# Performance work log

Hardware: AMD Instinct MI355X
Metric: run time of the kernel (lower is better)

## Reference

```python
import jax, jax.numpy as jnp
import numpy as np

N = 25000   # num nodes
E = 500000  # num edges
B = 4       # num queries (batch)
D = 32      # hidden dim
R2 = 474    # doubled num_relation
L = 4       # num conv layers
EPS = 1e-6


def setup_inputs() -> dict:
    key = jax.random.key(0)
    ks = jax.random.split(key, 12)
    return {
        "node_in": jax.random.randint(ks[0], (E,), 0, N),
        "node_out": jax.random.randint(ks[1], (E,), 0, N),
        "relation": jax.random.randint(ks[2], (E,), 0, R2),
        "edge_weight": jnp.ones((E,), jnp.float32),
        "h_index": jax.random.randint(ks[3], (B,), 0, N),
        "r_index": jax.random.randint(ks[4], (B,), 0, R2),
        "query_embed": jax.random.normal(ks[5], (R2, D), jnp.float32) * 0.1,
        "rel_W": jax.random.normal(ks[6], (L, D, R2 * D), jnp.float32) * 0.05,
        "rel_b": jnp.zeros((L, R2 * D), jnp.float32),
        "lin_W": jax.random.normal(ks[7], (L, 13 * D, D), jnp.float32) * 0.05,
        "lin_b": jnp.zeros((L, D), jnp.float32),
        "mlp_W1": jax.random.normal(ks[8], (2 * D, 2 * D), jnp.float32) * 0.05,
        "mlp_b1": jnp.zeros((2 * D,), jnp.float32),
        "mlp_W2": jax.random.normal(ks[9], (2 * D, 1), jnp.float32) * 0.05,
        "mlp_b2": jnp.zeros((1,), jnp.float32),
    }


def _nbfnet(node_in, node_out, relation, h_index, r_index,
            edge_weight, query_embed, rel_W, rel_b, lin_W, lin_b,
            mlp_W1, mlp_b1, mlp_W2, mlp_b2):
    query = query_embed[r_index]                                   # [B, D]
    # boundary condition: query embedding placed at the head node of each query
    boundary = jnp.zeros((N, B, D), query.dtype).at[h_index, jnp.arange(B)].set(query)
    # append one self-entry per node (boundary message), as in the torch code
    node_out_ext = jnp.concatenate([node_out, jnp.arange(N)])      # [E+N]
    w_ext = jnp.concatenate([edge_weight, jnp.ones((N,), edge_weight.dtype)])[:, None, None]
    cnt = jax.ops.segment_sum(jnp.ones((E + N,), query.dtype), node_out_ext, N)[:, None, None]
    deg = jax.ops.segment_sum(edge_weight, node_out, N) + 1.0      # degree_out + 1, [N]
    scale = jnp.log(deg)
    scale = scale / scale.mean()
    scales = jnp.stack([jnp.ones_like(scale), scale, 1.0 / jnp.clip(scale, 0.01)], -1)  # [N,3]

    hidden = boundary
    for l in range(L):
        # dependent relation embeddings: [R2, B, D]
        rel_in = (query @ rel_W[l] + rel_b[l]).reshape(B, R2, D).transpose(1, 0, 2)
        # distmult message + boundary self-message: [E+N, B, D]
        msg = jnp.concatenate([rel_in[relation] * hidden[node_in], boundary], 0)
        mw = msg * w_ext
        mean = jax.ops.segment_sum(mw, node_out_ext, N) / cnt
        sq_mean = jax.ops.segment_sum(msg * mw, node_out_ext, N) / cnt
        mx = jax.ops.segment_max(mw, node_out_ext, N)
        mn = jax.ops.segment_min(mw, node_out_ext, N)
        std = jnp.sqrt(jnp.clip(sq_mean - mean * mean, EPS))
        feat = jnp.stack([mean, mx, mn, std], -1).reshape(N, B, 4 * D)   # PNA stats
        update = (feat[..., None] * scales[:, None, None, :]).reshape(N, B, 12 * D)
        hidden = jax.nn.relu(jnp.concatenate([hidden, update], -1) @ lin_W[l] + lin_b[l])

    feat = jnp.concatenate([hidden, jnp.broadcast_to(query[None], (N, B, D))], -1)  # [N,B,2D]
    h1 = jax.nn.relu(feat @ mlp_W1 + mlp_b1)
    score = (h1 @ mlp_W2 + mlp_b2)[..., 0]                          # [N, B]
    return score.T                                                  # [B, N]


def reference(node_in, node_out, relation, edge_weight, h_index, r_index,
              query_embed, rel_W, rel_b, lin_W, lin_b,
              mlp_W1, mlp_b1, mlp_W2, mlp_b2):
    return _nbfnet(node_in, node_out, relation, h_index, r_index,
                   edge_weight, query_embed, rel_W, rel_b, lin_W, lin_b,
                   mlp_W1, mlp_b1, mlp_W2, mlp_b2)
```

## Files before the change

### kernel.cpp

```cpp
#include <hip/hip_runtime.h>
#include <hip/hip_fp16.h>

#define NN  25000
#define EE  500000
#define BB  4
#define DD  32
#define LL  4
#define R2C 474
#define BD  128
#define THD 416
#define EPSF 1e-6f
#define WMH 13312

typedef _Float16 half8 __attribute__((ext_vector_type(8)));
typedef float    f32x4 __attribute__((ext_vector_type(4)));

__global__ __launch_bounds__(256) void pidx_kernel(const int4* __restrict__ no4,
                                                   int* __restrict__ cnt,
                                                   int4* __restrict__ pidx4) {
  int i = blockIdx.x * 256 + threadIdx.x;
  if (i >= EE / 4) return;
  int4 d = no4[i];
  int4 r;
  r.x = atomicAdd(&cnt[d.x], 1);
  r.y = atomicAdd(&cnt[d.y], 1);
  r.z = atomicAdd(&cnt[d.z], 1);
  r.w = atomicAdd(&cnt[d.w], 1);
  pidx4[i] = r;
}

__global__ __launch_bounds__(256) void prep_kernel(const int* __restrict__ cnt,
                                                   int* __restrict__ base,
                                                   int* __restrict__ gcnt) {
  int n = blockIdx.x * 256 + threadIdx.x;
  if (n >= NN) return;
  base[n] = atomicAdd(gcnt, (cnt[n] + 1) & ~1);
}

__global__ __launch_bounds__(256) void scatter_kernel(const int4* __restrict__ ni4,
                                                      const int4* __restrict__ no4,
                                                      const int4* __restrict__ rl4,
                                                      const float4* __restrict__ ew4,
                                                      const int* __restrict__ base,
                                                      const int4* __restrict__ pidx4,
                                                      int2* __restrict__ ep) {
  int i = blockIdx.x * 256 + threadIdx.x;
  if (i >= EE / 4) return;
  int4 ni = ni4[i], no = no4[i], rl = rl4[i], pi = pidx4[i];
  float4 w = ew4[i];
  ep[base[no.x] + pi.x] = make_int2(ni.x | (rl.x << 15), __float_as_int(w.x));
  ep[base[no.y] + pi.y] = make_int2(ni.y | (rl.y << 15), __float_as_int(w.y));
  ep[base[no.z] + pi.z] = make_int2(ni.z | (rl.z << 15), __float_as_int(w.z));
  ep[base[no.w] + pi.w] = make_int2(ni.w | (rl.w << 15), __float_as_int(w.w));
}

__global__ __launch_bounds__(256) void wdeg_kernel(const int* __restrict__ base,
                                                   const int* __restrict__ cnt,
                                                   const int2* __restrict__ ep,
                                                   float* __restrict__ lg,
                                                   float* __restrict__ logsum) {
  int n = blockIdx.x * 256 + threadIdx.x;
  float v = 0.f;
  if (n < NN) {
    int b = base[n], c = cnt[n];
    float s = 0.f;
    for (int p = b; p < b + c; ++p) s += __int_as_float(ep[p].y);
    v = logf(s + 1.0f);
    lg[n] = v;
  }
  __shared__ float red[256];
  red[threadIdx.x] = v; __syncthreads();
  for (int o = 128; o > 0; o >>= 1) {
    if (threadIdx.x < o) red[threadIdx.x] += red[threadIdx.x + o];
    __syncthreads();
  }
  if (threadIdx.x == 0) atomicAdd(logsum, red[0]);
}

__global__ __launch_bounds__(128) void init_kernel(const int* __restrict__ r_index,
                                                   const float* __restrict__ qemb,
                                                   float* __restrict__ query) {
  int t = threadIdx.x; int b = t >> 5, d = t & 31;
  query[t] = qemb[r_index[b] * DD + d];
}

__global__ __launch_bounds__(256) void relin_all_kernel(const float* __restrict__ query,
                                                        const float* __restrict__ relW,
                                                        const float* __restrict__ relB,
                                                        __half* __restrict__ relIn) {
  int o = blockIdx.x * 256 + threadIdx.x;
  if (o >= LL * R2C * BD) return;
  int l = o / (R2C * BD);
  int rest = o % (R2C * BD);
  int r = rest >> 7, b = (rest >> 5) & 3, d = rest & 31;
  int col = r * DD + d;
  const float* W = relW + (size_t)l * DD * R2C * DD;
  float acc = relB[(size_t)l * R2C * DD + col];
  #pragma unroll
  for (int k = 0; k < DD; ++k)
    acc = fmaf(query[b * DD + k], W[(size_t)k * (R2C * DD) + col], acc);
  relIn[o] = __float2half(acc);
}

__global__ __launch_bounds__(256) void wmbuild_kernel(const float* __restrict__ linW,
                                                      _Float16* __restrict__ Wm) {
  int idx = blockIdx.x * 256 + threadIdx.x;
  if (idx >= LL * WMH) return;
  int l = idx / WMH, rest = idx % WMH;
  int t = rest >> 10;
  int nt = (rest >> 9) & 1;
  int L = (rest >> 3) & 63;
  int j = rest & 7;
  int k = t * 32 + (L >> 4) * 8 + j;
  int n = nt * 16 + (L & 15);
  int wrow;
  if (k < 32) wrow = k;
  else {
    int kk = k - 32;
    int slab = kk >> 7, s = (kk >> 5) & 3, dd = kk & 31;
    wrow = DD + (dd * 4 + s) * 3 + slab;
  }
  Wm[idx] = (_Float16)linW[(size_t)l * THD * DD + (size_t)wrow * DD + n];
}

__device__ __forceinline__ void mfma_epilogue(const _Float16* sh,
                                              const _Float16* hinh,
                                              __half* houth,
                                              const float* lg,
                                              const float* logsum,
                                              const _Float16* Wm,
                                              const float* bias,
                                              const float* query,
                                              const int* h_index,
                                              int nbase, int lane, bool hzero) {
  const int m = lane & 15;
  const int q = lane >> 4;
  const int nl = m >> 2;
  const int n = nbase + nl;
  const int b = m & 3;
  const float sc = lg[n] * ((float)NN / logsum[0]);
  const _Float16 one = (_Float16)1.f;
  const _Float16 s1h = (_Float16)sc;
  const _Float16 s2h = (_Float16)(1.0f / fmaxf(sc, 0.01f));
  const _Float16* ssrc = sh + nl * 512 + b * 32 + q * 8;

  f32x4 c0 = {0.f, 0.f, 0.f, 0.f};
  f32x4 c1 = {0.f, 0.f, 0.f, 0.f};
  half8 a;
  if (hzero) {
    a = (half8)(_Float16)0.f;
    if (n == h_index[b]) {
      const float* qp = query + b * 32 + q * 8;
      #pragma unroll
      for (int j = 0; j < 8; ++j) a[j] = (_Float16)qp[j];
    }
  } else {
    a = *(const half8*)(hinh + (unsigned)n * BD + b * 32 + q * 8);
  }
  #pragma unroll
  for (int t = 0; t < 13; ++t) {
    if (t > 0) {
      const int slab = (t - 1) >> 2, s = (t - 1) & 3;
      a = *(const half8*)(ssrc + s * 128);
      const _Float16 sch = (slab == 0) ? one : ((slab == 1) ? s1h : s2h);
      half8 sv = {sch, sch, sch, sch, sch, sch, sch, sch};
      a = a * sv;
    }
    half8 b0 = *(const half8*)(Wm + (unsigned)(t * 2 + 0) * 512 + lane * 8);
    half8 b1 = *(const half8*)(Wm + (unsigned)(t * 2 + 1) * 512 + lane * 8);
    c0 = __builtin_amdgcn_mfma_f32_16x16x32_f16(a, b0, c0, 0, 0, 0);
    c1 = __builtin_amdgcn_mfma_f32_16x16x32_f16(a, b1, c1, 0, 0, 0);
  }
  const int col = lane & 15;
  const float bj0 = bias[col], bj1 = bias[col + 16];
  #pragma unroll
  for (int i = 0; i < 4; ++i) {
    const int mr = q * 4 + i;
    __half* dst = houth + (unsigned)(nbase + (mr >> 2)) * BD + (mr & 3) * 32 + col;
    dst[0]  = __float2half(fmaxf(c0[i] + bj0, 0.f));
    dst[16] = __float2half(fmaxf(c1[i] + bj1, 0.f));
  }
}

__global__ __launch_bounds__(256) void layer1_fused_kernel(
    const __half2* __restrict__ rel2, const int2* __restrict__ ep,
    const int* __restrict__ base, const int* __restrict__ cnt,
    const int* __restrict__ h_index, const float* __restrict__ query,
    const float* __restrict__ lg, const float* __restrict__ logsum,
    const _Float16* __restrict__ Wm, const float* __restrict__ bias,
    __half* __restrict__ houth) {
  __shared__ __align__(16) __half2 sh[4][256];
  const int lane = threadIdx.x & 63;
  const int wid  = threadIdx.x >> 6;
  const int nbase = blockIdx.x * 4;
  const int n = nbase + wid;
  const int b = lane >> 4;
  const int d0 = (lane & 15) * 2;
  const float q0 = query[b * 32 + d0], q1 = query[b * 32 + d0 + 1];
  const int hb = h_index[b];
  const int beg = __builtin_amdgcn_readfirstlane(base[n]);
  const int cnn = __builtin_amdgcn_readfirstlane(cnt[n]);
  const float mb0 = (n == hb) ? q0 : 0.f;
  const float mb1 = (n == hb) ? q1 : 0.f;
  float sa0 = mb0, qa0 = mb0 * mb0, mx0 = mb0, mn0 = mb0;
  float sa1 = mb1, qa1 = mb1 * mb1, mx1 = mb1, mn1 = mb1;
  int matched = 0;
  for (int p = beg; p < beg + cnn; ++p) {
    int2 e = ep[p];
    if ((e.x & 0x7fff) == hb) {
      __half2 rv = rel2[(unsigned)((unsigned)e.x >> 15) * 64 + lane];
      float w = __int_as_float(e.y);
      float2 rf = __half22float2(rv);
      float m0 = rf.x * q0, mw0 = m0 * w;
      float m1 = rf.y * q1, mw1 = m1 * w;
      sa0 += mw0; qa0 = fmaf(m0, mw0, qa0); mx0 = fmaxf(mx0, mw0); mn0 = fminf(mn0, mw0);
      sa1 += mw1; qa1 = fmaf(m1, mw1, qa1); mx1 = fmaxf(mx1, mw1); mn1 = fminf(mn1, mw1);
      ++matched;
    }
  }
  if (matched < cnn) {
    mx0 = fmaxf(mx0, 0.f); mn0 = fminf(mn0, 0.f);
    mx1 = fmaxf(mx1, 0.f); mn1 = fminf(mn1, 0.f);
  }
  const float invc = 1.0f / (float)(cnn + 1);
  const float mean0 = sa0 * invc, mean1 = sa1 * invc;
  const float sd0 = sqrtf(fmaxf(qa0 * invc - mean0 * mean0, EPSF));
  const float sd1 = sqrtf(fmaxf(qa1 * invc - mean1 * mean1, EPSF));
  sh[wid][lane]       = __floats2half2_rn(mean0, mean1);
  sh[wid][64 + lane]  = __floats2half2_rn(mx0, mx1);
  sh[wid][128 + lane] = __floats2half2_rn(mn0, mn1);
  sh[wid][192 + lane] = __floats2half2_rn(sd0, sd1);
  __syncthreads();
  if (threadIdx.x >= 64) return;
  mfma_epilogue((const _Float16*)&sh[0][0], nullptr, houth, lg, logsum,
                Wm, bias, query, h_index, nbase, lane, true);
}

__global__ __launch_bounds__(256) void layer_fused_kernel(
    const __half2* __restrict__ hin2, const __half2* __restrict__ rel2,
    const int2* __restrict__ ep, const int* __restrict__ base,
    const int* __restrict__ cnt, const int* __restrict__ h_index,
    const float* __restrict__ query, const float* __restrict__ lg,
    const float* __restrict__ logsum, const _Float16* __restrict__ Wm,
    const float* __restrict__ bias, __half* __restrict__ houth) {
  __shared__ __align__(16) __half2 sh[4][256];
  const int lane = threadIdx.x & 63;
  const int wid  = threadIdx.x >> 6;
  const int nbase = blockIdx.x * 4;
  const int n = nbase + wid;
  const int b = lane >> 4;
  const int d0 = (lane & 15) * 2;
  const float q0 = query[b * 32 + d0], q1 = query[b * 32 + d0 + 1];
  const int hb = h_index[b];
  const int beg = __builtin_amdgcn_readfirstlane(base[n]);
  const int cnn = __builtin_amdgcn_readfirstlane(cnt[n]);
  const float mb0 = (n == hb) ? q0 : 0.f;
  const float mb1 = (n == hb) ? q1 : 0.f;
  float sa0 = mb0, qa0 = mb0 * mb0, mx0 = mb0, mn0 = mb0;
  float sa1 = mb1, qa1 = mb1 * mb1, mx1 = mb1, mn1 = mb1;

#define PROC(Ez, Hv, Rv) {                                                   \
    float w = __int_as_float(Ez);                                            \
    float2 hf = __half22float2(Hv), rf = __half22float2(Rv);                 \
    float m0 = rf.x * hf.x, mw0 = m0 * w;                                    \
    float m1 = rf.y * hf.y, mw1 = m1 * w;                                    \
    sa0 += mw0; qa0 = fmaf(m0, mw0, qa0);                                    \
    mx0 = fmaxf(mx0, mw0); mn0 = fminf(mn0, mw0);                            \
    sa1 += mw1; qa1 = fmaf(m1, mw1, qa1);                                    \
    mx1 = fmaxf(mx1, mw1); mn1 = fminf(mn1, mw1); }
#define ROWS(Ex, Hd, Rd) {                                                   \
    Hd = hin2[(unsigned)((Ex) & 0x7fff) * 64 + lane];                        \
    Rd = rel2[(unsigned)((unsigned)(Ex) >> 15) * 64 + lane]; }

  int p = beg;
  int rem = cnn;
  const int nb = rem >> 3;
  if (nb > 0) {
    int2 E0, E1, E2, E3, E4, E5, E6, E7;
    __half2 H0, H1, H2, H3, H4, H5, H6, H7;
    __half2 R0, R1, R2, R3, R4, R5, R6, R7;
    E0 = ep[p];     E1 = ep[p + 1]; E2 = ep[p + 2]; E3 = ep[p + 3];
    E4 = ep[p + 4]; E5 = ep[p + 5]; E6 = ep[p + 6]; E7 = ep[p + 7];
    ROWS(E0.x, H0, R0); ROWS(E1.x, H1, R1); ROWS(E2.x, H2, R2); ROWS(E3.x, H3, R3);
    ROWS(E4.x, H4, R4); ROWS(E5.x, H5, R5); ROWS(E6.x, H6, R6); ROWS(E7.x, H7, R7);
    for (int it = 1; it < nb; ++it) {
      const int pn = p + 8;
      int2 F0 = ep[pn],     F1 = ep[pn + 1], F2 = ep[pn + 2], F3 = ep[pn + 3];
      int2 F4 = ep[pn + 4], F5 = ep[pn + 5], F6 = ep[pn + 6], F7 = ep[pn + 7];
      __half2 G0, G1, G2, G3, G4, G5, G6, G7;
      __half2 S0, S1, S2, S3, S4, S5, S6, S7;
      ROWS(F0.x, G0, S0); ROWS(F1.x, G1, S1); ROWS(F2.x, G2, S2); ROWS(F3.x, G3, S3);
      ROWS(F4.x, G4, S4); ROWS(F5.x, G5, S5); ROWS(F6.x, G6, S6); ROWS(F7.x, G7, S7);
      PROC(E0.y, H0, R0); PROC(E1.y, H1, R1); PROC(E2.y, H2, R2); PROC(E3.y, H3, R3);
      PROC(E4.y, H4, R4); PROC(E5.y, H5, R5); PROC(E6.y, H6, R6); PROC(E7.y, H7, R7);
      E0 = F0; E1 = F1; E2 = F2; E3 = F3; E4 = F4; E5 = F5; E6 = F6; E7 = F7;
      H0 = G0; H1 = G1; H2 = G2; H3 = G3; H4 = G4; H5 = G5; H6 = G6; H7 = G7;
      R0 = S0; R1 = S1; R2 = S2; R3 = S3; R4 = S4; R5 = S5; R6 = S6; R7 = S7;
      p = pn;
    }
    PROC(E0.y, H0, R0); PROC(E1.y, H1, R1); PROC(E2.y, H2, R2); PROC(E3.y, H3, R3);
    PROC(E4.y, H4, R4); PROC(E5.y, H5, R5); PROC(E6.y, H6, R6); PROC(E7.y, H7, R7);
    p += 8;
    rem -= nb << 3;
  }
  if (rem >= 4) {
    int2 E0 = ep[p], E1 = ep[p + 1], E2 = ep[p + 2], E3 = ep[p + 3];
    __half2 H0, H1, H2, H3, R0, R1, R2, R3;
    ROWS(E0.x, H0, R0); ROWS(E1.x, H1, R1); ROWS(E2.x, H2, R2); ROWS(E3.x, H3, R3);
    PROC(E0.y, H0, R0); PROC(E1.y, H1, R1); PROC(E2.y, H2, R2); PROC(E3.y, H3, R3);
    p += 4; rem -= 4;
  }
  for (; rem > 0; --rem, ++p) {
    int2 e = ep[p];
    __half2 hv, rv;
    ROWS(e.x, hv, rv);
    PROC(e.y, hv, rv);
  }
#undef ROWS
#undef PROC
  const float invc = 1.0f / (float)(cnn + 1);
  const float mean0 = sa0 * invc, mean1 = sa1 * invc;
  const float sd0 = sqrtf(fmaxf(qa0 * invc - mean0 * mean0, EPSF));
  const float sd1 = sqrtf(fmaxf(qa1 * invc - mean1 * mean1, EPSF));
  sh[wid][lane]       = __floats2half2_rn(mean0, mean1);
  sh[wid][64 + lane]  = __floats2half2_rn(mx0, mx1);
  sh[wid][128 + lane] = __floats2half2_rn(mn0, mn1);
  sh[wid][192 + lane] = __floats2half2_rn(sd0, sd1);
  __syncthreads();
  if (threadIdx.x >= 64) return;
  mfma_epilogue((const _Float16*)&sh[0][0], (const _Float16*)hin2, houth,
                lg, logsum, Wm, bias, query, h_index, nbase, lane, false);
}

__global__ __launch_bounds__(128) void mlp_kernel(const __half* __restrict__ hinh,
                                                  const float* __restrict__ query,
                                                  const float* __restrict__ W1,
                                                  const float* __restrict__ b1,
                                                  const float* __restrict__ W2,
                                                  const float* __restrict__ b2,
                                                  float* __restrict__ out) {
  __shared__ float f2[BB][2 * DD];
  const int t = threadIdx.x;
  const int b = t >> 5, d = t & 31;
  const float qv = query[t];
  const float w2a = W2[d], w2b = W2[DD + d];
  const float b1a = b1[d], b1b = b1[DD + d];
  const float b2v = b2[0];
  const int NPBM = 8;
  int n0 = blockIdx.x * NPBM, n1 = min(n0 + NPBM, NN);
  for (int n = n0; n < n1; ++n) {
    f2[b][d]      = __half2float(hinh[(unsigned)n * BD + t]);
    f2[b][DD + d] = qv;
    float a0 = b1a, a1 = b1b;
    #pragma unroll
    for (int i = 0; i < 2 * DD; ++i) {
      float v = f2[b][i];
      a0 = fmaf(v, W1[i * 2 * DD + d], a0);
      a1 = fmaf(v, W1[i * 2 * DD + DD + d], a1);
    }
    a0 = fmaxf(a0, 0.f); a1 = fmaxf(a1, 0.f);
    float part = a0 * w2a + a1 * w2b;
    #pragma unroll
    for (int off = 16; off > 0; off >>= 1) part += __shfl_down(part, off, 32);
    if (d == 0) out[b * NN + n] = part + b2v;
  }
}

extern "C" void kernel_launch(void* const* d_in, const int* in_sizes, int n_in,
                              void* d_out, int out_size, void* d_ws, size_t ws_size,
                              hipStream_t stream) {
  const int*   node_in  = (const int*)d_in[0];
  const int*   node_out = (const int*)d_in[1];
  const int*   relation = (const int*)d_in[2];
  const float* ew       = (const float*)d_in[3];
  const int*   h_index  = (const int*)d_in[4];
  const int*   r_index  = (const int*)d_in[5];
  const float* qemb     = (const float*)d_in[6];
  const float* relW     = (const float*)d_in[7];
  const float* relB     = (const float*)d_in[8];
  const float* linW     = (const float*)d_in[9];
  const float* linB     = (const float*)d_in[10];
  const float* W1       = (const float*)d_in[11];
  const float* b1       = (const float*)d_in[12];
  const float* W2       = (const float*)d_in[13];
  const float* b2       = (const float*)d_in[14];
  float* out = (float*)d_out;

  char* ws = (char*)d_ws;
  size_t off = 0;
  auto alloc = [&](size_t bytes) -> char* {
    char* p = ws + off;
    off += (bytes + 255) & ~(size_t)255;
    return p;
  };
  __half*   h0     = (__half*)  alloc((size_t)NN * BD * 2);
  __half*   h1     = (__half*)  alloc((size_t)NN * BD * 2);
  __half*   relIn  = (__half*)  alloc((size_t)LL * R2C * BD * 2);
  _Float16* Wm     = (_Float16*)alloc((size_t)LL * WMH * 2);
  int2*     ep     = (int2*)    alloc(((size_t)EE + NN) * 8);
  int*      pidx   = (int*)     alloc((size_t)EE * 4);
  int*      base   = (int*)     alloc((size_t)NN * 4);
  int*      cnti   = (int*)     alloc((size_t)NN * 4);
  float*    lg     = (float*)   alloc((size_t)NN * 4);
  float*    query  = (float*)   alloc((size_t)BD * 4);
  float*    stats  = (float*)   alloc(256);

  hipMemsetAsync(cnti, 0, (size_t)NN * 4, stream);
  hipMemsetAsync(stats, 0, 256, stream);

  float* logsum = stats;
  int*   gcnt   = (int*)stats + 1;

  pidx_kernel   <<<(EE / 4 + 255) / 256, 256, 0, stream>>>((const int4*)node_out,
                                                           cnti, (int4*)pidx);
  prep_kernel   <<<(NN + 255) / 256, 256, 0, stream>>>(cnti, base, gcnt);
  scatter_kernel<<<(EE / 4 + 255) / 256, 256, 0, stream>>>(
      (const int4*)node_in, (const int4*)node_out, (const int4*)relation,
      (const float4*)ew, base, (const int4*)pidx, ep);
  wdeg_kernel   <<<(NN + 255) / 256, 256, 0, stream>>>(base, cnti, ep, lg, logsum);
  init_kernel   <<<1, 128, 0, stream>>>(r_index, qemb, query);
  wmbuild_kernel<<<(LL * WMH + 255) / 256, 256, 0, stream>>>(linW, Wm);
  relin_all_kernel<<<(LL * R2C * BD + 255) / 256, 256, 0, stream>>>(query, relW, relB, relIn);

  __half* hin = h0; __half* hout = h1;
  for (int l = 0; l < LL; ++l) {
    if (l == 0) {
      layer1_fused_kernel<<<NN / 4, 256, 0, stream>>>(
          (const __half2*)relIn, ep, base, cnti, h_index, query, lg, logsum,
          Wm, linB, hout);
    } else {
      layer_fused_kernel<<<NN / 4, 256, 0, stream>>>(
          (const __half2*)hin, (const __half2*)relIn + (size_t)l * R2C * 64,
          ep, base, cnti, h_index, query, lg, logsum,
          Wm + (size_t)l * WMH, linB + (size_t)l * DD, hout);
    }
    __half* tmp = hin; hin = hout; hout = tmp;
  }
  mlp_kernel<<<(NN + 7) / 8, 128, 0, stream>>>(hin, query, W1, b1, W2, b2, out);
}
```

Baseline: 287.7 us.

## Fuse setup kernels and fold final MLP into last layer epilogue via MFMA

Weighted degree is now accumulated with float atomics during the counting pass, so the separate degree kernel that re-read the CSR edge list is gone. Scatter, weight repacking, relation projection, query init and a new packed W1 build are merged into one multi-role launch. The final MLP runs inside the last layer's epilogue using MFMA instead of a separate scalar kernel, which avoids writing and re-reading the last hidden state. The trade-offs are extra atomics, half-precision MLP inputs, and extra shared memory in every layer launch.

```diff
diff --git a/kernel.cpp b/kernel.cpp
--- a/kernel.cpp
+++ b/kernel.cpp
@@ -12,60 +12,46 @@
 #define EPSF 1e-6f
 #define WMH 13312
 
+#define NSCAT  489
+#define NWMB   208
+#define NRELIN 948
+#define NW1P   16
+
 typedef _Float16 half8 __attribute__((ext_vector_type(8)));
 typedef float    f32x4 __attribute__((ext_vector_type(4)));
 
 __global__ __launch_bounds__(256) void pidx_kernel(const int4* __restrict__ no4,
+                                                   const float4* __restrict__ ew4,
                                                    int* __restrict__ cnt,
+                                                   float* __restrict__ wsum,
                                                    int4* __restrict__ pidx4) {
   int i = blockIdx.x * 256 + threadIdx.x;
   if (i >= EE / 4) return;
   int4 d = no4[i];
+  float4 w = ew4[i];
   int4 r;
   r.x = atomicAdd(&cnt[d.x], 1);
   r.y = atomicAdd(&cnt[d.y], 1);
   r.z = atomicAdd(&cnt[d.z], 1);
   r.w = atomicAdd(&cnt[d.w], 1);
+  atomicAdd(&wsum[d.x], w.x);
+  atomicAdd(&wsum[d.y], w.y);
+  atomicAdd(&wsum[d.z], w.z);
+  atomicAdd(&wsum[d.w], w.w);
   pidx4[i] = r;
 }
 
 __global__ __launch_bounds__(256) void prep_kernel(const int* __restrict__ cnt,
+                                                   const float* __restrict__ wsum,
                                                    int* __restrict__ base,
-                                                   int* __restrict__ gcnt) {
-  int n = blockIdx.x * 256 + threadIdx.x;
-  if (n >= NN) return;
-  base[n] = atomicAdd(gcnt, (cnt[n] + 1) & ~1);
-}
-
-__global__ __launch_bounds__(256) void scatter_kernel(const int4* __restrict__ ni4,
-                                                      const int4* __restrict__ no4,
-                                                      const int4* __restrict__ rl4,
-                                                      const float4* __restrict__ ew4,
-                                                      const int* __restrict__ base,
-                                                      const int4* __restrict__ pidx4,
-                                                      int2* __restrict__ ep) {
-  int i = blockIdx.x * 256 + threadIdx.x;
-  if (i >= EE / 4) return;
-  int4 ni = ni4[i], no = no4[i], rl = rl4[i], pi = pidx4[i];
-  float4 w = ew4[i];
-  ep[base[no.x] + pi.x] = make_int2(ni.x | (rl.x << 15), __float_as_int(w.x));
-  ep[base[no.y] + pi.y] = make_int2(ni.y | (rl.y << 15), __float_as_int(w.y));
-  ep[base[no.z] + pi.z] = make_int2(ni.z | (rl.z << 15), __float_as_int(w.z));
-  ep[base[no.w] + pi.w] = make_int2(ni.w | (rl.w << 15), __float_as_int(w.w));
-}
-
-__global__ __launch_bounds__(256) void wdeg_kernel(const int* __restrict__ base,
-                                                   const int* __restrict__ cnt,
-                                                   const int2* __restrict__ ep,
+                                                   int* __restrict__ gcnt,
                                                    float* __restrict__ lg,
                                                    float* __restrict__ logsum) {
   int n = blockIdx.x * 256 + threadIdx.x;
   float v = 0.f;
   if (n < NN) {
-    int b = base[n], c = cnt[n];
-    float s = 0.f;
-    for (int p = b; p < b + c; ++p) s += __int_as_float(ep[p].y);
-    v = logf(s + 1.0f);
+    base[n] = atomicAdd(gcnt, (cnt[n] + 1) & ~1);
+    v = logf(wsum[n] + 1.0f);
     lg[n] = v;
   }
   __shared__ float red[256];
@@ -77,52 +63,72 @@
   if (threadIdx.x == 0) atomicAdd(logsum, red[0]);
 }
 
-__global__ __launch_bounds__(128) void init_kernel(const int* __restrict__ r_index,
-                                                   const float* __restrict__ qemb,
-                                                   float* __restrict__ query) {
-  int t = threadIdx.x; int b = t >> 5, d = t & 31;
-  query[t] = qemb[r_index[b] * DD + d];
-}
-
-__global__ __launch_bounds__(256) void relin_all_kernel(const float* __restrict__ query,
-                                                        const float* __restrict__ relW,
-                                                        const float* __restrict__ relB,
-                                                        __half* __restrict__ relIn) {
-  int o = blockIdx.x * 256 + threadIdx.x;
-  if (o >= LL * R2C * BD) return;
-  int l = o / (R2C * BD);
-  int rest = o % (R2C * BD);
-  int r = rest >> 7, b = (rest >> 5) & 3, d = rest & 31;
-  int col = r * DD + d;
-  const float* W = relW + (size_t)l * DD * R2C * DD;
-  float acc = relB[(size_t)l * R2C * DD + col];
-  #pragma unroll
-  for (int k = 0; k < DD; ++k)
-    acc = fmaf(query[b * DD + k], W[(size_t)k * (R2C * DD) + col], acc);
-  relIn[o] = __float2half(acc);
-}
-
-__global__ __launch_bounds__(256) void wmbuild_kernel(const float* __restrict__ linW,
-                                                      _Float16* __restrict__ Wm) {
-  int idx = blockIdx.x * 256 + threadIdx.x;
-  if (idx >= LL * WMH) return;
-  int l = idx / WMH, rest = idx % WMH;
-  int t = rest >> 10;
-  int nt = (rest >> 9) & 1;
-  int L = (rest >> 3) & 63;
-  int j = rest & 7;
-  int k = t * 32 + (L >> 4) * 8 + j;
-  int n = nt * 16 + (L & 15);
-  int wrow;
-  if (k < 32) wrow = k;
-  else {
-    int kk = k - 32;
-    int slab = kk >> 7, s = (kk >> 5) & 3, dd = kk & 31;
-    wrow = DD + (dd * 4 + s) * 3 + slab;
-  }
-  Wm[idx] = (_Float16)linW[(size_t)l * THD * DD + (size_t)wrow * DD + n];
-}
-
+__global__ __launch_bounds__(256) void scatter_setup_kernel(
+    const int4* __restrict__ ni4, const int4* __restrict__ no4,
+    const int4* __restrict__ rl4, const float4* __restrict__ ew4,
+    const int* __restrict__ base, const int4* __restrict__ pidx4,
+    int2* __restrict__ ep,
+    const float* __restrict__ linW, _Float16* __restrict__ Wm,
+    const int* __restrict__ r_index, const float* __restrict__ qemb,
+    const float* __restrict__ relW, const float* __restrict__ relB,
+    __half* __restrict__ relIn, float* __restrict__ query,
+    const float* __restrict__ W1, _Float16* __restrict__ W1m) {
+  const int blk = blockIdx.x;
+  const int tid = threadIdx.x;
+  if (blk < NSCAT) {
+    int i = blk * 256 + tid;
+    if (i >= EE / 4) return;
+    int4 ni = ni4[i], no = no4[i], rl = rl4[i], pi = pidx4[i];
+    float4 w = ew4[i];
+    ep[base[no.x] + pi.x] = make_int2(ni.x | (rl.x << 15), __float_as_int(w.x));
+    ep[base[no.y] + pi.y] = make_int2(ni.y | (rl.y << 15), __float_as_int(w.y));
+    ep[base[no.z] + pi.z] = make_int2(ni.z | (rl.z << 15), __float_as_int(w.z));
+    ep[base[no.w] + pi.w] = make_int2(ni.w | (rl.w << 15), __float_as_int(w.w));
+  } else if (blk < NSCAT + NWMB) {
+    int idx = (blk - NSCAT) * 256 + tid;
+    int l = idx / WMH, rest = idx % WMH;
+    int t = rest >> 10;
+    int nt = (rest >> 9) & 1;
+    int L = (rest >> 3) & 63;
+    int j = rest & 7;
+    int k = t * 32 + (L >> 4) * 8 + j;
+    int n = nt * 16 + (L & 15);
+    int wrow;
+    if (k < 32) wrow = k;
+    else {
+      int kk = k - 32;
+      int slab = kk >> 7, s = (kk >> 5) & 3, dd = kk & 31;
+      wrow = DD + (dd * 4 + s) * 3 + slab;
+    }
+    Wm[idx] = (_Float16)linW[(size_t)l * THD * DD + (size_t)wrow * DD + n];
+  } else if (blk < NSCAT + NWMB + NRELIN) {
+    int o = (blk - NSCAT - NWMB) * 256 + tid;
+    int l = o / (R2C * BD);
+    int rest = o % (R2C * BD);
+    int r = rest >> 7, b = (rest >> 5) & 3, d = rest & 31;
+    int col = r * DD + d;
+    const float* W = relW + (size_t)l * DD * R2C * DD;
+    const float* qrow = qemb + (size_t)r_index[b] * DD;
+    float acc = relB[(size_t)l * R2C * DD + col];
+    #pragma unroll
+    for (int k = 0; k < DD; ++k)
+      acc = fmaf(qrow[k], W[(size_t)k * (R2C * DD) + col], acc);
+    relIn[o] = __float2half(acc);
+  } else if (blk < NSCAT + NWMB + NRELIN + NW1P) {
+    int idx = (blk - NSCAT - NWMB - NRELIN) * 256 + tid;
+    int kc = idx >> 11;
+    int nt = (idx >> 9) & 3;
+    int L = (idx >> 3) & 63;
+    int j = idx & 7;
+    int k = kc * 32 + (L >> 4) * 8 + j;
+    int c = nt * 16 + (L & 15);
+    W1m[idx] = (_Float16)W1[(size_t)k * (2 * DD) + c];
+  } else {
+    if (tid < BD) query[tid] = qemb[(size_t)r_index[tid >> 5] * DD + (tid & 31)];
+  }
+}
+
+template <bool LAST>
 __device__ __forceinline__ void mfma_epilogue(const _Float16* sh,
                                               const _Float16* hinh,
                                               __half* houth,
@@ -132,7 +138,13 @@
                                               const float* bias,
                                               const float* query,
                                               const int* h_index,
-                                              int nbase, int lane, bool hzero) {
+                                              int nbase, int lane, bool hzero,
+                                              const _Float16* W1m,
+                                              const float* b1,
+                                              const float* W2,
+                                              const float* b2,
+                                              float* out,
+                                              _Float16* hbuf) {
   const int m = lane & 15;
   const int q = lane >> 4;
   const int nl = m >> 2;
@@ -167,18 +179,65 @@
       a = a * sv;
     }
     half8 b0 = *(const half8*)(Wm + (unsigned)(t * 2 + 0) * 512 + lane * 8);
-    half8 b1 = *(const half8*)(Wm + (unsigned)(t * 2 + 1) * 512 + lane * 8);
+    half8 b1f = *(const half8*)(Wm + (unsigned)(t * 2 + 1) * 512 + lane * 8);
     c0 = __builtin_amdgcn_mfma_f32_16x16x32_f16(a, b0, c0, 0, 0, 0);
-    c1 = __builtin_amdgcn_mfma_f32_16x16x32_f16(a, b1, c1, 0, 0, 0);
+    c1 = __builtin_amdgcn_mfma_f32_16x16x32_f16(a, b1f, c1, 0, 0, 0);
   }
   const int col = lane & 15;
   const float bj0 = bias[col], bj1 = bias[col + 16];
-  #pragma unroll
-  for (int i = 0; i < 4; ++i) {
-    const int mr = q * 4 + i;
-    __half* dst = houth + (unsigned)(nbase + (mr >> 2)) * BD + (mr & 3) * 32 + col;
-    dst[0]  = __float2half(fmaxf(c0[i] + bj0, 0.f));
-    dst[16] = __float2half(fmaxf(c1[i] + bj1, 0.f));
+  if constexpr (!LAST) {
+    #pragma unroll
+    for (int i = 0; i < 4; ++i) {
+      const int mr = q * 4 + i;
+      __half* dst = houth + (unsigned)(nbase + (mr >> 2)) * BD + (mr & 3) * 32 + col;
+      dst[0]  = __float2half(fmaxf(c0[i] + bj0, 0.f));
+      dst[16] = __float2half(fmaxf(c1[i] + bj1, 0.f));
+    }
+  } else {
+    #pragma unroll
+    for (int i = 0; i < 4; ++i) {
+      const int mr = q * 4 + i;
+      hbuf[mr * 32 + col]      = (_Float16)fmaxf(c0[i] + bj0, 0.f);
+      hbuf[mr * 32 + 16 + col] = (_Float16)fmaxf(c1[i] + bj1, 0.f);
+    }
+    half8 ah = *(const half8*)(hbuf + m * 32 + q * 8);
+    half8 aq;
+    const float* qp = query + b * 32 + q * 8;
+    #pragma unroll
+    for (int j = 0; j < 8; ++j) aq[j] = (_Float16)qp[j];
+    f32x4 h1c[4];
+    #pragma unroll
+    for (int nt = 0; nt < 4; ++nt) {
+      h1c[nt] = (f32x4){0.f, 0.f, 0.f, 0.f};
+      half8 w0 = *(const half8*)(W1m + (unsigned)(0 * 4 + nt) * 512 + lane * 8);
+      half8 w1 = *(const half8*)(W1m + (unsigned)(1 * 4 + nt) * 512 + lane * 8);
+      h1c[nt] = __builtin_amdgcn_mfma_f32_16x16x32_f16(ah, w0, h1c[nt], 0, 0, 0);
+      h1c[nt] = __builtin_amdgcn_mfma_f32_16x16x32_f16(aq, w1, h1c[nt], 0, 0, 0);
+    }
+    float part[4] = {0.f, 0.f, 0.f, 0.f};
+    #pragma unroll
+    for (int nt = 0; nt < 4; ++nt) {
+      const float bb = b1[nt * 16 + col];
+      const float ww = W2[nt * 16 + col];
+      #pragma unroll
+      for (int i = 0; i < 4; ++i) {
+        float v = fmaxf(h1c[nt][i] + bb, 0.f);
+        part[i] = fmaf(v, ww, part[i]);
+      }
+    }
+    #pragma unroll
+    for (int i = 0; i < 4; ++i) {
+      part[i] += __shfl_xor(part[i], 1);
+      part[i] += __shfl_xor(part[i], 2);
+      part[i] += __shfl_xor(part[i], 4);
+      part[i] += __shfl_xor(part[i], 8);
+    }
+    if (col == 0) {
+      const float b2v = b2[0];
+      #pragma unroll
+      for (int i = 0; i < 4; ++i)
+        out[(unsigned)i * NN + nbase + q] = part[i] + b2v;
+    }
   }
 }
 
@@ -232,18 +291,24 @@
   sh[wid][192 + lane] = __floats2half2_rn(sd0, sd1);
   __syncthreads();
   if (threadIdx.x >= 64) return;
-  mfma_epilogue((const _Float16*)&sh[0][0], nullptr, houth, lg, logsum,
-                Wm, bias, query, h_index, nbase, lane, true);
-}
-
+  mfma_epilogue<false>((const _Float16*)&sh[0][0], nullptr, houth, lg, logsum,
+                       Wm, bias, query, h_index, nbase, lane, true,
+                       nullptr, nullptr, nullptr, nullptr, nullptr, nullptr);
+}
+
+template <bool LAST>
 __global__ __launch_bounds__(256) void layer_fused_kernel(
     const __half2* __restrict__ hin2, const __half2* __restrict__ rel2,
     const int2* __restrict__ ep, const int* __restrict__ base,
     const int* __restrict__ cnt, const int* __restrict__ h_index,
     const float* __restrict__ query, const float* __restrict__ lg,
     const float* __restrict__ logsum, const _Float16* __restrict__ Wm,
-    const float* __restrict__ bias, __half* __restrict__ houth) {
+    const float* __restrict__ bias, __half* __restrict__ houth,
+    const _Float16* __restrict__ W1m, const float* __restrict__ b1,
+    const float* __restrict__ W2, const float* __restrict__ b2,
+    float* __restrict__ out) {
   __shared__ __align__(16) __half2 sh[4][256];
+  __shared__ __align__(16) _Float16 hbuf[512];
   const int lane = threadIdx.x & 63;
   const int wid  = threadIdx.x >> 6;
   const int nbase = blockIdx.x * 4;
@@ -328,42 +393,9 @@
   sh[wid][192 + lane] = __floats2half2_rn(sd0, sd1);
   __syncthreads();
   if (threadIdx.x >= 64) return;
-  mfma_epilogue((const _Float16*)&sh[0][0], (const _Float16*)hin2, houth,
-                lg, logsum, Wm, bias, query, h_index, nbase, lane, false);
-}
-
-__global__ __launch_bounds__(128) void mlp_kernel(const __half* __restrict__ hinh,
-                                                  const float* __restrict__ query,
-                                                  const float* __restrict__ W1,
-                                                  const float* __restrict__ b1,
-                                                  const float* __restrict__ W2,
-                                                  const float* __restrict__ b2,
-                                                  float* __restrict__ out) {
-  __shared__ float f2[BB][2 * DD];
-  const int t = threadIdx.x;
-  const int b = t >> 5, d = t & 31;
-  const float qv = query[t];
-  const float w2a = W2[d], w2b = W2[DD + d];
-  const float b1a = b1[d], b1b = b1[DD + d];
-  const float b2v = b2[0];
-  const int NPBM = 8;
-  int n0 = blockIdx.x * NPBM, n1 = min(n0 + NPBM, NN);
-  for (int n = n0; n < n1; ++n) {
-    f2[b][d]      = __half2float(hinh[(unsigned)n * BD + t]);
-    f2[b][DD + d] = qv;
-    float a0 = b1a, a1 = b1b;
-    #pragma unroll
-    for (int i = 0; i < 2 * DD; ++i) {
-      float v = f2[b][i];
-      a0 = fmaf(v, W1[i * 2 * DD + d], a0);
-      a1 = fmaf(v, W1[i * 2 * DD + DD + d], a1);
-    }
-    a0 = fmaxf(a0, 0.f); a1 = fmaxf(a1, 0.f);
-    float part = a0 * w2a + a1 * w2b;
-    #pragma unroll
-    for (int off = 16; off > 0; off >>= 1) part += __shfl_down(part, off, 32);
-    if (d == 0) out[b * NN + n] = part + b2v;
-  }
+  mfma_epilogue<LAST>((const _Float16*)&sh[0][0], (const _Float16*)hin2, houth,
+                      lg, logsum, Wm, bias, query, h_index, nbase, lane, false,
+                      W1m, b1, W2, b2, out, hbuf);
 }
 
 extern "C" void kernel_launch(void* const* d_in, const int* in_sizes, int n_in,
@@ -394,47 +426,54 @@
     return p;
   };
   __half*   h0     = (__half*)  alloc((size_t)NN * BD * 2);
-  __half*   h1     = (__half*)  alloc((size_t)NN * BD * 2);
+  __half*   h1buf  = (__half*)  alloc((size_t)NN * BD * 2);
   __half*   relIn  = (__half*)  alloc((size_t)LL * R2C * BD * 2);
   _Float16* Wm     = (_Float16*)alloc((size_t)LL * WMH * 2);
+  _Float16* W1m    = (_Float16*)alloc((size_t)4096 * 2);
   int2*     ep     = (int2*)    alloc(((size_t)EE + NN) * 8);
   int*      pidx   = (int*)     alloc((size_t)EE * 4);
+  int*      cw     = (int*)     alloc((size_t)NN * 8);
   int*      base   = (int*)     alloc((size_t)NN * 4);
-  int*      cnti   = (int*)     alloc((size_t)NN * 4);
   float*    lg     = (float*)   alloc((size_t)NN * 4);
   float*    query  = (float*)   alloc((size_t)BD * 4);
   float*    stats  = (float*)   alloc(256);
 
-  hipMemsetAsync(cnti, 0, (size_t)NN * 4, stream);
+  int*   cnti = cw;
+  float* wsum = (float*)(cw + NN);
+
+  hipMemsetAsync(cw, 0, (size_t)NN * 8, stream);
   hipMemsetAsync(stats, 0, 256, stream);
 
   float* logsum = stats;
   int*   gcnt   = (int*)stats + 1;
 
-  pidx_kernel   <<<(EE / 4 + 255) / 256, 256, 0, stream>>>((const int4*)node_out,
-                                                           cnti, (int4*)pidx);
-  prep_kernel   <<<(NN + 255) / 256, 256, 0, stream>>>(cnti, base, gcnt);
-  scatter_kernel<<<(EE / 4 + 255) / 256, 256, 0, stream>>>(
+  pidx_kernel<<<(EE / 4 + 255) / 256, 256, 0, stream>>>(
+      (const int4*)node_out, (const float4*)ew, cnti, wsum, (int4*)pidx);
+  prep_kernel<<<(NN + 255) / 256, 256, 0, stream>>>(cnti, wsum, base, gcnt, lg, logsum);
+  scatter_setup_kernel<<<NSCAT + NWMB + NRELIN + NW1P + 1, 256, 0, stream>>>(
       (const int4*)node_in, (const int4*)node_out, (const int4*)relation,
-      (const float4*)ew, base, (const int4*)pidx, ep);
-  wdeg_kernel   <<<(NN + 255) / 256, 256, 0, stream>>>(base, cnti, ep, lg, logsum);
-  init_kernel   <<<1, 128, 0, stream>>>(r_index, qemb, query);
-  wmbuild_kernel<<<(LL * WMH + 255) / 256, 256, 0, stream>>>(linW, Wm);
-  relin_all_kernel<<<(LL * R2C * BD + 255) / 256, 256, 0, stream>>>(query, relW, relB, relIn);
-
-  __half* hin = h0; __half* hout = h1;
+      (const float4*)ew, base, (const int4*)pidx, ep,
+      linW, Wm, r_index, qemb, relW, relB, relIn, query, W1, W1m);
+
+  __half* hin = h0; __half* hout = h1buf;
   for (int l = 0; l < LL; ++l) {
     if (l == 0) {
       layer1_fused_kernel<<<NN / 4, 256, 0, stream>>>(
           (const __half2*)relIn, ep, base, cnti, h_index, query, lg, logsum,
           Wm, linB, hout);
-    } else {
-      layer_fused_kernel<<<NN / 4, 256, 0, stream>>>(
+    } else if (l < LL - 1) {
+      layer_fused_kernel<false><<<NN / 4, 256, 0, stream>>>(
           (const __half2*)hin, (const __half2*)relIn + (size_t)l * R2C * 64,
           ep, base, cnti, h_index, query, lg, logsum,
-          Wm + (size_t)l * WMH, linB + (size_t)l * DD, hout);
+          Wm + (size_t)l * WMH, linB + (size_t)l * DD, hout,
+          nullptr, nullptr, nullptr, nullptr, nullptr);
+    } else {
+      layer_fused_kernel<true><<<NN / 4, 256, 0, stream>>>(
+          (const __half2*)hin, (const __half2*)relIn + (size_t)l * R2C * 64,
+          ep, base, cnti, h_index, query, lg, logsum,
+          Wm + (size_t)l * WMH, linB + (size_t)l * DD, hout,
+          W1m, b1, W2, b2, out);
     }
     __half* tmp = hin; hin = hout; hout = tmp;
   }
-  mlp_kernel<<<(NN + 7) / 8, 128, 0, stream>>>(hin, query, W1, b1, W2, b2, out);
-}
+}
```

Measured after the change: 281.5 us. -2.2%, faster.
